# Kernel optimization log

Measured on AMD Instinct MI355X. Metric: run time of the kernel, lower is better.

## Reference

```python
import jax, jax.numpy as jnp
import numpy as np

BATCH = 16384
EPS = 1e-5


def _pool22_sum(x):
    # 4 * AvgPool2d((2,2),stride 2) == sum over 2x2 blocks. x: [B,1,h,w]
    B, C, h, w = x.shape
    return x.reshape(B, C, h // 2, 2, w // 2, 2).sum(axis=(3, 5))


def _transform(img, ans):
    # img: [B,h,h]. Faithful port of `transfrom`: zero border rows/cols, then
    # 10 quadratic features per 2x2 patch, laid out as [B,1,k,10k] with last
    # axis index = patch_col*10 + feature.
    B, h, w = img.shape
    if ans in ('top_bottom', 'all'):
        m = jnp.ones((h, 1), img.dtype).at[0].set(0).at[-1].set(0)
        img = img * m
    if ans in ('left_right', 'all'):
        m = jnp.ones((1, w), img.dtype).at[:, 0].set(0).at[:, -1].set(0)
        img = img * m
    k = h // 2
    p = img.reshape(B, k, 2, k, 2)
    b00 = p[:, :, 0, :, 0]; b01 = p[:, :, 0, :, 1]
    b10 = p[:, :, 1, :, 0]; b11 = p[:, :, 1, :, 1]
    prods = jnp.stack([
        b00 * b00, b01 * b01, b10 * b10, b11 * b11,
        b00 * b01, b00 * b10, b00 * b11,
        b01 * b10, b01 * b11, b10 * b11], axis=-1)  # [B,k,k,10]
    return prods.reshape(B, 1, k, 10 * k)


def _pool110_sum(a):
    # 10 * AvgPool2d((1,10),stride(1,10)) == sum over groups of 10 on last axis
    B, C, k, tk = a.shape
    return a.reshape(B, C, k, tk // 10, 10).sum(-1)


def _bn(x, gamma, beta):
    # BatchNorm2d(1) in training mode: batch stats over (N,H,W), biased var
    m = x.mean(axis=(0, 2, 3), keepdims=True)
    v = jnp.mean((x - m) ** 2, axis=(0, 2, 3), keepdims=True)
    g = gamma.reshape(1, -1, 1, 1)
    b = beta.reshape(1, -1, 1, 1)
    return (x - m) * jax.lax.rsqrt(v + EPS) * g + b


def setup_inputs() -> dict:
    key = jax.random.key(0)
    ks = jax.random.split(key, 16)

    def xavier(k, shape):
        fan_in, fan_out = shape[-1], shape[-2]
        std = np.sqrt(2.0 / (fan_in + fan_out))
        return jax.random.normal(k, shape, jnp.float32) * std

    return {
        'x': jax.random.normal(ks[0], (BATCH, 1, 28, 28), jnp.float32),
        'l1_w1': xavier(ks[1], (1, 28, 28)),
        'l1_w2_1': xavier(ks[2], (1, 14, 140)),
        'l1_w2_2': xavier(ks[3], (1, 14, 140)),
        'l1_w2_3': xavier(ks[4], (1, 14, 140)),
        'l1_w2_4': xavier(ks[5], (1, 14, 140)),
        'l1_w3': xavier(ks[6], (1, 14, 14)),
        'l2_w1': xavier(ks[7], (1, 14, 14)),
        'l2_w2': xavier(ks[8], (1, 7, 70)),
        'l2_w4': xavier(ks[9], (1, 7, 7)),
        'w_fc1': jax.random.normal(ks[10], (10, 49), jnp.float32) / np.sqrt(49.0),
        'b_fc1': jnp.zeros((10,), jnp.float32),
        'w_fc2': jax.random.normal(ks[11], (10, 2401), jnp.float32) / np.sqrt(2401.0),
        'b_fc2': jnp.zeros((10,), jnp.float32),
        'bn_gamma': jnp.ones((1,), jnp.float32),
        'bn_beta': jnp.zeros((1,), jnp.float32),
    }


def reference(x, l1_w1, l1_w2_1, l1_w2_2, l1_w2_3, l1_w2_4, l1_w3,
              l2_w1, l2_w2, l2_w4, w_fc1, b_fc1, w_fc2, b_fc2,
              bn_gamma, bn_beta):
    B = x.shape[0]
    img = x[:, 0]  # [B,28,28]
    # layer 1
    l1 = _pool22_sum(x * l1_w1)
    for W, ans in ((l1_w2_1, 'left_right'), (l1_w2_2, 'top_bottom'),
                   (l1_w2_3, 'all'), (l1_w2_4, 'none')):
        l1 = l1 + _pool110_sum(_transform(img, ans) * W)
    l1 = l1 + l1_w3  # [B,1,14,14]
    h = _bn(l1, bn_gamma, bn_beta)
    # layer 2
    l2 = _pool22_sum(h * l2_w1) + _pool110_sum(_transform(h[:, 0], 'none') * l2_w2) + l2_w4
    h = _bn(l2, bn_gamma, bn_beta)  # [B,1,7,7]
    # layer 3
    l3_x1 = h.reshape(B, -1) @ w_fc1.T + b_fc1
    v = h.reshape(B, 49)
    c = jnp.triu(v[:, :, None] * v[:, None, :])  # [B,49,49], trans_all_rg
    l3_x2 = c.reshape(B, -1) @ w_fc2.T + b_fc2
    return l3_x1 + l3_x2
```

## Files before the change

kernel.cpp:

```cpp
#include <hip/hip_runtime.h>

#define BATCH 16384
#define N1 (BATCH * 196)
#define N2 (BATCH * 49)
#define S1 8

#define WS_P1_OFF   0
#define WS_P2_OFF   32768
#define WS_W2S_OFF  65536
#define WS_L1G_OFF  262144
#define WS_L2G_OFF  6684672

__device__ __forceinline__ unsigned short f2bf(float f) {
    unsigned u = __float_as_uint(f);
    unsigned r = (u + 0x7FFFu + ((u >> 16) & 1u)) >> 16;
    return (unsigned short)r;
}
__device__ __forceinline__ float bf2f(unsigned short h) {
    return __uint_as_float((unsigned)h << 16);
}

__global__ void __launch_bounds__(256) k1(
        const float* __restrict__ x,
        const float* __restrict__ l1w1, const float* __restrict__ wA,
        const float* __restrict__ wB, const float* __restrict__ wC,
        const float* __restrict__ wD, const float* __restrict__ l1w3,
        const float* __restrict__ wf2, const float* __restrict__ wfc1,
        const float* __restrict__ bfc1, const float* __restrict__ bfc2,
        unsigned short* __restrict__ l1g, double* __restrict__ partials1,
        float* __restrict__ w2s) {
    __shared__ __align__(16) float xs[S1 * 784];
    __shared__ float wls[4], wlss[4];
    int t = threadIdx.x;

    const float4* src = (const float4*)(x + (size_t)blockIdx.x * (S1 * 784));
    float4 rbuf[6];
    #pragma unroll
    for (int i = 0; i < 6; ++i) rbuf[i] = src[t + 256 * i];
    float4 rtail;
    if (t < 32) rtail = src[t + 1536];

    bool active = t < 196;
    int pos = active ? t : 0;
    int pi = pos / 14, pj = pos - 14 * pi;
    int r0 = (2 * pi) * 28 + 2 * pj;
    float4 a0, a1, a2, a3;
    {
        float2 wt = *(const float2*)(l1w1 + r0);
        float2 wb = *(const float2*)(l1w1 + r0 + 28);
        a0 = make_float4(wt.x, wt.y, wb.x, wb.y);
        float mA0 = (pj != 0) ? 1.f : 0.f, mA1 = (pj != 13) ? 1.f : 0.f;
        float mB0 = (pi != 0) ? 1.f : 0.f, mB1 = (pi != 13) ? 1.f : 0.f;
        float eA[4] = {mA0, mA1, mA0, mA1};
        float eB[4] = {mB0, mB0, mB1, mB1};
        const int e1i[10] = {0,1,2,3,0,0,0,1,1,2};
        const int e2i[10] = {0,1,2,3,1,2,3,2,3,3};
        int wo = pi * 140 + 10 * pj;
        float wq[10];
        #pragma unroll
        for (int k = 0; k < 10; ++k) {
            float ca = eA[e1i[k]] * eA[e2i[k]];
            float cb = eB[e1i[k]] * eB[e2i[k]];
            wq[k] = wA[wo + k] * ca + wB[wo + k] * cb
                  + wC[wo + k] * ca * cb + wD[wo + k];
        }
        a1 = make_float4(wq[0], wq[1], wq[2], wq[3]);
        a2 = make_float4(wq[4], wq[5], wq[6], wq[7]);
        a3 = make_float4(wq[8], wq[9], l1w3[pos], 0.f);
    }

    float4* dst = (float4*)xs;
    #pragma unroll
    for (int i = 0; i < 6; ++i) dst[t + 256 * i] = rbuf[i];
    if (t < 32) dst[t + 1536] = rtail;
    __syncthreads();

    float accs[S1];
    float sum = 0.f, sumsq = 0.f;
    #pragma unroll
    for (int s = 0; s < S1; ++s) {
        const float* xb = xs + s * 784;
        float2 tp = *(const float2*)(xb + r0);
        float2 bo = *(const float2*)(xb + r0 + 28);
        float b00 = tp.x, b01 = tp.y, b10 = bo.x, b11 = bo.y;
        float acc = b00 * a0.x + b01 * a0.y + b10 * a0.z + b11 * a0.w;
        acc += b00 * b00 * a1.x + b01 * b01 * a1.y + b10 * b10 * a1.z + b11 * b11 * a1.w;
        acc += b00 * b01 * a2.x + b00 * b10 * a2.y + b00 * b11 * a2.z + b01 * b10 * a2.w;
        acc += b01 * b11 * a3.x + b10 * b11 * a3.y + a3.z;
        accs[s] = acc;
        if (active) { sum += acc; sumsq += acc * acc; }
    }

    __syncthreads();
    unsigned short* ob = (unsigned short*)xs;
    if (active) {
        int g = ((pi >> 1) * 7 + (pj >> 1)) * 4 + (pi & 1) * 2 + (pj & 1);
        #pragma unroll
        for (int s = 0; s < S1; ++s) ob[s * 196 + g] = f2bf(accs[s]);
    }
    __syncthreads();
    const unsigned int* ob32 = (const unsigned int*)ob;
    unsigned int* gout = (unsigned int*)(l1g + (size_t)blockIdx.x * (S1 * 196));
    #pragma unroll
    for (int r2 = 0; r2 < 3; ++r2) gout[t + 256 * r2] = ob32[t + 256 * r2];
    if (t < 16) gout[t + 768] = ob32[t + 768];

    #pragma unroll
    for (int off = 32; off; off >>= 1) {
        sum += __shfl_down(sum, off);
        sumsq += __shfl_down(sumsq, off);
    }
    int lane = t & 63, wid = t >> 6;
    if (lane == 0) { wls[wid] = sum; wlss[wid] = sumsq; }
    __syncthreads();
    if (t == 0) {
        partials1[blockIdx.x * 2]     = (double)(wls[0] + wls[1] + wls[2] + wls[3]);
        partials1[blockIdx.x * 2 + 1] = (double)(wlss[0] + wlss[1] + wlss[2] + wlss[3]);
    }

    if (blockIdx.x < 10) {
        int e = blockIdx.x * 256 + t;
        if (e < 2500) {
            int p = e / 50, q = e - 50 * p;
            float w[10];
            if (p < 49 && q < 49) {
                int lo = p < q ? p : q, hi = p < q ? q : p;
                float sc = (p == q) ? 1.f : 0.5f;
                #pragma unroll
                for (int o = 0; o < 10; ++o) w[o] = wf2[o * 2401 + lo * 49 + hi] * sc;
            } else if (p == 49 && q < 49) {
                #pragma unroll
                for (int o = 0; o < 10; ++o) w[o] = wfc1[o * 49 + q];
            } else if (p < 49) {
                #pragma unroll
                for (int o = 0; o < 10; ++o) w[o] = 0.f;
            } else {
                #pragma unroll
                for (int o = 0; o < 10; ++o) w[o] = bfc1[o] + bfc2[o];
            }
            #pragma unroll
            for (int o = 0; o < 10; ++o) w2s[e * 10 + o] = w[o];
        }
    }
}

__global__ void __launch_bounds__(256) k2(
        const unsigned short* __restrict__ l1g,
        const float* __restrict__ l2w1, const float* __restrict__ l2w2,
        const float* __restrict__ l2w4,
        const float* __restrict__ gamma, const float* __restrict__ beta,
        const double* __restrict__ partials1, double* __restrict__ partials2,
        float* __restrict__ l2g) {
    __shared__ float wls[4], wlss[4];
    __shared__ double dred[8];
    __shared__ float bcast[2];
    int t = threadIdx.x;
    int lane = t & 63, wid = t >> 6;
    int sbase = blockIdx.x * S1;

    bool active = t < 196;
    int tt = active ? t : 0;
    int sub = tt / 49;
    int pos = tt - 49 * sub;

    ushort4 u0 = *(const ushort4*)(l1g + ((size_t)(sbase + sub) * 49 + pos) * 4);
    ushort4 u1 = *(const ushort4*)(l1g + ((size_t)(sbase + 4 + sub) * 49 + pos) * 4);

    {
        double s = 0.0, ss = 0.0;
        const double* p1 = partials1 + t * 16;
        #pragma unroll
        for (int k = 0; k < 8; ++k) { s += p1[k * 2]; ss += p1[k * 2 + 1]; }
        #pragma unroll
        for (int off = 32; off; off >>= 1) {
            s += __shfl_down(s, off);
            ss += __shfl_down(ss, off);
        }
        if (lane == 0) { dred[wid * 2] = s; dred[wid * 2 + 1] = ss; }
        __syncthreads();
        if (t == 0) {
            double S = dred[0] + dred[2] + dred[4] + dred[6];
            double SS = dred[1] + dred[3] + dred[5] + dred[7];
            double mean = S / (double)N1;
            double var = SS / (double)N1 - mean * mean;
            float a = (float)((double)gamma[0] / sqrt(var + 1e-5));
            bcast[0] = a;
            bcast[1] = beta[0] - (float)mean * a;
        }
    }

    int pi = pos / 7, pj = pos - 7 * pi;
    int r0 = (2 * pi) * 14 + 2 * pj;
    float4 a0 = make_float4(l2w1[r0], l2w1[r0 + 1], l2w1[r0 + 14], l2w1[r0 + 15]);
    int wo = pi * 70 + 10 * pj;
    float4 q1 = make_float4(l2w2[wo],     l2w2[wo + 1], l2w2[wo + 2], l2w2[wo + 3]);
    float4 q2 = make_float4(l2w2[wo + 4], l2w2[wo + 5], l2w2[wo + 6], l2w2[wo + 7]);
    float4 q3 = make_float4(l2w2[wo + 8], l2w2[wo + 9], l2w4[pos], 0.f);
    __syncthreads();
    float a1 = bcast[0], c1 = bcast[1];

    float sum = 0.f, sumsq = 0.f;
    #pragma unroll
    for (int s2 = 0; s2 < 2; ++s2) {
        ushort4 u = s2 ? u1 : u0;
        int smp = sbase + s2 * 4 + sub;
        float h00 = fmaf(a1, bf2f(u.x), c1), h01 = fmaf(a1, bf2f(u.y), c1);
        float h10 = fmaf(a1, bf2f(u.z), c1), h11 = fmaf(a1, bf2f(u.w), c1);
        float acc = h00 * a0.x + h01 * a0.y + h10 * a0.z + h11 * a0.w;
        acc += h00 * h00 * q1.x + h01 * h01 * q1.y + h10 * h10 * q1.z + h11 * h11 * q1.w;
        acc += h00 * h01 * q2.x + h00 * h10 * q2.y + h00 * h11 * q2.z + h01 * h10 * q2.w;
        acc += h01 * h11 * q3.x + h10 * h11 * q3.y + q3.z;
        if (active) {
            l2g[(size_t)smp * 52 + pos] = acc;
            sum += acc;
            sumsq += acc * acc;
        }
    }

    #pragma unroll
    for (int off = 32; off; off >>= 1) {
        sum += __shfl_down(sum, off);
        sumsq += __shfl_down(sumsq, off);
    }
    if (lane == 0) { wls[wid] = sum; wlss[wid] = sumsq; }
    __syncthreads();
    if (t == 0) {
        partials2[blockIdx.x * 2]     = (double)(wls[0] + wls[1] + wls[2] + wls[3]);
        partials2[blockIdx.x * 2 + 1] = (double)(wlss[0] + wlss[1] + wlss[2] + wlss[3]);
    }
}

__global__ void __launch_bounds__(1024) k3(
        const float* __restrict__ l2g, const float* __restrict__ w2s,
        const float* __restrict__ gamma, const float* __restrict__ beta,
        const double* __restrict__ partials2, float* __restrict__ out) {
    __shared__ float part[16][64][10];
    __shared__ double dred[32];
    __shared__ float bcast[2];
    int t = threadIdx.x, lane = t & 63, wid = t >> 6;
    int s = blockIdx.x * 64 + lane;

    float v[52];
    const float4* vsrc = (const float4*)(l2g + (size_t)s * 52);
    #pragma unroll
    for (int k = 0; k < 13; ++k) *(float4*)(v + 4 * k) = vsrc[k];

    {
        const double* p2 = partials2 + t * 4;
        double sd = p2[0] + p2[2], ssd = p2[1] + p2[3];
        #pragma unroll
        for (int off = 32; off; off >>= 1) {
            sd += __shfl_down(sd, off);
            ssd += __shfl_down(ssd, off);
        }
        if (lane == 0) { dred[wid * 2] = sd; dred[wid * 2 + 1] = ssd; }
        __syncthreads();
        if (t == 0) {
            double S = 0.0, SS = 0.0;
            #pragma unroll
            for (int w = 0; w < 16; ++w) { S += dred[w * 2]; SS += dred[w * 2 + 1]; }
            double mean = S / (double)N2;
            double var = SS / (double)N2 - mean * mean;
            float a = (float)((double)gamma[0] / sqrt(var + 1e-5));
            bcast[0] = a;
            bcast[1] = beta[0] - (float)mean * a;
        }
        __syncthreads();
    }
    float a2 = bcast[0], c2 = bcast[1];
    #pragma unroll
    for (int k = 0; k < 49; ++k) v[k] = fmaf(a2, v[k], c2);
    v[49] = 1.f;

    float acc[10];
    #pragma unroll
    for (int o = 0; o < 10; ++o) acc[o] = 0.f;

    int W = __builtin_amdgcn_readfirstlane(wid);
    for (int r = W; r < 50; r += 16) {
        float vp = (r < 49) ? fmaf(a2, l2g[(size_t)s * 52 + r], c2) : 1.f;
        const float* wr = w2s + r * 500;
        #pragma unroll
        for (int q = 0; q < 50; ++q) {
            float c = vp * v[q];
            #pragma unroll
            for (int o = 0; o < 10; ++o) acc[o] = fmaf(c, wr[q * 10 + o], acc[o]);
        }
    }

    #pragma unroll
    for (int o = 0; o < 10; ++o) part[wid][lane][o] = acc[o];
    __syncthreads();

    if (t < 640) {
        int sl = t / 10, o = t - 10 * sl;
        float r2 = 0.f;
        #pragma unroll
        for (int w = 0; w < 16; ++w) r2 += part[w][sl][o];
        out[(size_t)(blockIdx.x * 64 + sl) * 10 + o] = r2;
    }
}

extern "C" void kernel_launch(void* const* d_in, const int* in_sizes, int n_in,
                              void* d_out, int out_size, void* d_ws, size_t ws_size,
                              hipStream_t stream) {
    const float* x       = (const float*)d_in[0];
    const float* l1_w1   = (const float*)d_in[1];
    const float* l1_w2_1 = (const float*)d_in[2];
    const float* l1_w2_2 = (const float*)d_in[3];
    const float* l1_w2_3 = (const float*)d_in[4];
    const float* l1_w2_4 = (const float*)d_in[5];
    const float* l1_w3   = (const float*)d_in[6];
    const float* l2_w1   = (const float*)d_in[7];
    const float* l2_w2   = (const float*)d_in[8];
    const float* l2_w4   = (const float*)d_in[9];
    const float* w_fc1   = (const float*)d_in[10];
    const float* b_fc1   = (const float*)d_in[11];
    const float* w_fc2   = (const float*)d_in[12];
    const float* b_fc2   = (const float*)d_in[13];
    const float* bn_gamma = (const float*)d_in[14];
    const float* bn_beta  = (const float*)d_in[15];

    char* ws = (char*)d_ws;
    double* partials1 = (double*)(ws + WS_P1_OFF);
    double* partials2 = (double*)(ws + WS_P2_OFF);
    float* w2s = (float*)(ws + WS_W2S_OFF);
    unsigned short* l1g = (unsigned short*)(ws + WS_L1G_OFF);
    float* l2g = (float*)(ws + WS_L2G_OFF);
    float* out = (float*)d_out;

    k1<<<BATCH / S1, 256, 0, stream>>>(x, l1_w1, l1_w2_1, l1_w2_2, l1_w2_3, l1_w2_4,
                                       l1_w3, w_fc2, w_fc1, b_fc1, b_fc2,
                                       l1g, partials1, w2s);
    k2<<<BATCH / S1, 256, 0, stream>>>(l1g, l2_w1, l2_w2, l2_w4, bn_gamma, bn_beta,
                                       partials1, partials2, l2g);
    k3<<<BATCH / 64, 1024, 0, stream>>>(l2g, w2s, bn_gamma, bn_beta, partials2, out);
}
```

Measured before the change: 48.34 us.

## Use upper-triangular pair stream with compile-time indices in FC2 kernel

The FC2 quadratic layer previously iterated over a full symmetrized 50x50 pair matrix (with halved off-diagonal weights plus a bias row and column). It now iterates only the 1225 upper-triangular (p,q) pairs, with weights pre-packed per wave into a contiguous stream. The pair indices are resolved at compile time via templates, so each wave indexes registers statically. FC1 and the bias are handled separately, removing roughly half of the FMAs. The cost is a 16-way switch over template instantiations that greatly enlarges code size, which may pressure the instruction cache.

```diff
diff --git a/kernel.cpp b/kernel.cpp
--- a/kernel.cpp
+++ b/kernel.cpp
@@ -4,12 +4,14 @@
 #define N1 (BATCH * 196)
 #define N2 (BATCH * 49)
 #define S1 8
-
-#define WS_P1_OFF   0
-#define WS_P2_OFF   32768
-#define WS_W2S_OFF  65536
-#define WS_L1G_OFF  262144
-#define WS_L2G_OFF  6684672
+#define NPART 16
+
+#define WS_P1_OFF    0
+#define WS_P2_OFF    32768
+#define WS_WSTR_OFF  65536
+#define WS_WFC1S_OFF 114816
+#define WS_L1G_OFF   262144
+#define WS_L2G_OFF   6684672
 
 __device__ __forceinline__ unsigned short f2bf(float f) {
     unsigned u = __float_as_uint(f);
@@ -18,6 +20,17 @@
 }
 __device__ __forceinline__ float bf2f(unsigned short h) {
     return __uint_as_float((unsigned)h << 16);
+}
+
+__host__ __device__ constexpr int pair_p(int i) {
+    int p = 0, rem = i;
+    while (rem >= 49 - p) { rem -= 49 - p; ++p; }
+    return p;
+}
+__host__ __device__ constexpr int pair_q(int i) {
+    int p = 0, rem = i;
+    while (rem >= 49 - p) { rem -= 49 - p; ++p; }
+    return p + rem;
 }
 
 __global__ void __launch_bounds__(256) k1(
@@ -26,9 +39,8 @@
         const float* __restrict__ wB, const float* __restrict__ wC,
         const float* __restrict__ wD, const float* __restrict__ l1w3,
         const float* __restrict__ wf2, const float* __restrict__ wfc1,
-        const float* __restrict__ bfc1, const float* __restrict__ bfc2,
         unsigned short* __restrict__ l1g, double* __restrict__ partials1,
-        float* __restrict__ w2s) {
+        float* __restrict__ wstream, float* __restrict__ wfc1s) {
     __shared__ __align__(16) float xs[S1 * 784];
     __shared__ float wls[4], wlss[4];
     int t = threadIdx.x;
@@ -120,26 +132,17 @@
 
     if (blockIdx.x < 10) {
         int e = blockIdx.x * 256 + t;
-        if (e < 2500) {
-            int p = e / 50, q = e - 50 * p;
-            float w[10];
-            if (p < 49 && q < 49) {
-                int lo = p < q ? p : q, hi = p < q ? q : p;
-                float sc = (p == q) ? 1.f : 0.5f;
-                #pragma unroll
-                for (int o = 0; o < 10; ++o) w[o] = wf2[o * 2401 + lo * 49 + hi] * sc;
-            } else if (p == 49 && q < 49) {
-                #pragma unroll
-                for (int o = 0; o < 10; ++o) w[o] = wfc1[o * 49 + q];
-            } else if (p < 49) {
-                #pragma unroll
-                for (int o = 0; o < 10; ++o) w[o] = 0.f;
-            } else {
-                #pragma unroll
-                for (int o = 0; o < 10; ++o) w[o] = bfc1[o] + bfc2[o];
-            }
+        if (e < 1225) {
+            int rem = e, p = 0;
+            while (rem >= 49 - p) { rem -= 49 - p; ++p; }
+            int q = p + rem;
+            int slot = ((e & (NPART - 1)) * 77 + (e / NPART)) * 10;
             #pragma unroll
-            for (int o = 0; o < 10; ++o) w2s[e * 10 + o] = w[o];
+            for (int o = 0; o < 10; ++o) wstream[slot + o] = wf2[o * 2401 + p * 49 + q];
+        } else if (e < 1274) {
+            int k = e - 1225;
+            #pragma unroll
+            for (int o = 0; o < 10; ++o) wfc1s[k * 10 + o] = wfc1[o * 49 + k];
         }
     }
 }
@@ -230,11 +233,43 @@
     }
 }
 
+template<int W, int J>
+__device__ __forceinline__ void fc2_steps(const float* __restrict__ wb,
+                                          const float* v, float* acc) {
+    constexpr int i = J * NPART + W;
+    if constexpr (i < 1225) {
+        constexpr int p = pair_p(i);
+        constexpr int q = pair_q(i);
+        float pv = v[p] * v[q];
+        const float* w = wb + J * 10;
+        #pragma unroll
+        for (int o = 0; o < 10; ++o) acc[o] = fmaf(pv, w[o], acc[o]);
+        fc2_steps<W, J + 1>(wb, v, acc);
+    }
+}
+
+template<int W>
+__device__ __forceinline__ void fc_all(const float* __restrict__ wstream,
+                                       const float* __restrict__ wfc1s,
+                                       const float* v, float* acc) {
+    #pragma unroll
+    for (int k = 0; k < 49; ++k) {
+        if ((k & (NPART - 1)) == W) {
+            const float* w = wfc1s + k * 10;
+            #pragma unroll
+            for (int o = 0; o < 10; ++o) acc[o] = fmaf(v[k], w[o], acc[o]);
+        }
+    }
+    fc2_steps<W, 0>(wstream + W * 770, v, acc);
+}
+
 __global__ void __launch_bounds__(1024) k3(
-        const float* __restrict__ l2g, const float* __restrict__ w2s,
+        const float* __restrict__ l2g, const float* __restrict__ wstream,
+        const float* __restrict__ wfc1s,
+        const float* __restrict__ b_fc1, const float* __restrict__ b_fc2,
         const float* __restrict__ gamma, const float* __restrict__ beta,
         const double* __restrict__ partials2, float* __restrict__ out) {
-    __shared__ float part[16][64][10];
+    __shared__ float part[NPART][64][10];
     __shared__ double dred[32];
     __shared__ float bcast[2];
     int t = threadIdx.x, lane = t & 63, wid = t >> 6;
@@ -270,22 +305,29 @@
     float a2 = bcast[0], c2 = bcast[1];
     #pragma unroll
     for (int k = 0; k < 49; ++k) v[k] = fmaf(a2, v[k], c2);
-    v[49] = 1.f;
 
     float acc[10];
     #pragma unroll
     for (int o = 0; o < 10; ++o) acc[o] = 0.f;
 
     int W = __builtin_amdgcn_readfirstlane(wid);
-    for (int r = W; r < 50; r += 16) {
-        float vp = (r < 49) ? fmaf(a2, l2g[(size_t)s * 52 + r], c2) : 1.f;
-        const float* wr = w2s + r * 500;
-        #pragma unroll
-        for (int q = 0; q < 50; ++q) {
-            float c = vp * v[q];
-            #pragma unroll
-            for (int o = 0; o < 10; ++o) acc[o] = fmaf(c, wr[q * 10 + o], acc[o]);
-        }
+    switch (W) {
+        case 0:  fc_all<0>(wstream, wfc1s, v, acc); break;
+        case 1:  fc_all<1>(wstream, wfc1s, v, acc); break;
+        case 2:  fc_all<2>(wstream, wfc1s, v, acc); break;
+        case 3:  fc_all<3>(wstream, wfc1s, v, acc); break;
+        case 4:  fc_all<4>(wstream, wfc1s, v, acc); break;
+        case 5:  fc_all<5>(wstream, wfc1s, v, acc); break;
+        case 6:  fc_all<6>(wstream, wfc1s, v, acc); break;
+        case 7:  fc_all<7>(wstream, wfc1s, v, acc); break;
+        case 8:  fc_all<8>(wstream, wfc1s, v, acc); break;
+        case 9:  fc_all<9>(wstream, wfc1s, v, acc); break;
+        case 10: fc_all<10>(wstream, wfc1s, v, acc); break;
+        case 11: fc_all<11>(wstream, wfc1s, v, acc); break;
+        case 12: fc_all<12>(wstream, wfc1s, v, acc); break;
+        case 13: fc_all<13>(wstream, wfc1s, v, acc); break;
+        case 14: fc_all<14>(wstream, wfc1s, v, acc); break;
+        default: fc_all<15>(wstream, wfc1s, v, acc); break;
     }
 
     #pragma unroll
@@ -296,8 +338,8 @@
         int sl = t / 10, o = t - 10 * sl;
         float r2 = 0.f;
         #pragma unroll
-        for (int w = 0; w < 16; ++w) r2 += part[w][sl][o];
-        out[(size_t)(blockIdx.x * 64 + sl) * 10 + o] = r2;
+        for (int w = 0; w < NPART; ++w) r2 += part[w][sl][o];
+        out[(size_t)(blockIdx.x * 64 + sl) * 10 + o] = r2 + b_fc1[o] + b_fc2[o];
     }
 }
 
@@ -324,15 +366,17 @@
     char* ws = (char*)d_ws;
     double* partials1 = (double*)(ws + WS_P1_OFF);
     double* partials2 = (double*)(ws + WS_P2_OFF);
-    float* w2s = (float*)(ws + WS_W2S_OFF);
+    float* wstream = (float*)(ws + WS_WSTR_OFF);
+    float* wfc1s   = (float*)(ws + WS_WFC1S_OFF);
     unsigned short* l1g = (unsigned short*)(ws + WS_L1G_OFF);
     float* l2g = (float*)(ws + WS_L2G_OFF);
     float* out = (float*)d_out;
 
     k1<<<BATCH / S1, 256, 0, stream>>>(x, l1_w1, l1_w2_1, l1_w2_2, l1_w2_3, l1_w2_4,
-                                       l1_w3, w_fc2, w_fc1, b_fc1, b_fc2,
-                                       l1g, partials1, w2s);
+                                       l1_w3, w_fc2, w_fc1, l1g, partials1,
+                                       wstream, wfc1s);
     k2<<<BATCH / S1, 256, 0, stream>>>(l1g, l2_w1, l2_w2, l2_w4, bn_gamma, bn_beta,
                                        partials1, partials2, l2g);
-    k3<<<BATCH / 64, 1024, 0, stream>>>(l2g, w2s, bn_gamma, bn_beta, partials2, out);
-}
+    k3<<<BATCH / 64, 1024, 0, stream>>>(l2g, wstream, wfc1s, b_fc1, b_fc2,
+                                        bn_gamma, bn_beta, partials2, out);
+}
```

New measurement: 51.39 us, median of 2. +6.3%, slower.

## Exploit upper-triangular structure in FC2 with packed pair records and LDS activations

Applied to the files above, without the earlier changes.

Replaces the dense 50x50 symmetric weight sweep in k3 with a list of 1274 upper-triangle (p,q) pair records, each holding 10 weights plus precomputed LDS offsets, split round-robin across 16 waves. Per-sample normalized activations now sit in shared memory in a transposed layout rather than in 52 registers. This roughly halves the FMA work and cuts register pressure. In exchange it adds two LDS reads and scalar readfirstlane loads per record, and moves the bias add to the final output write.

```diff
diff --git a/kernel.cpp b/kernel.cpp
--- a/kernel.cpp
+++ b/kernel.cpp
@@ -4,12 +4,13 @@
 #define N1 (BATCH * 196)
 #define N2 (BATCH * 49)
 #define S1 8
-
-#define WS_P1_OFF   0
-#define WS_P2_OFF   32768
-#define WS_W2S_OFF  65536
-#define WS_L1G_OFF  262144
-#define WS_L2G_OFF  6684672
+#define NREC 80
+
+#define WS_P1_OFF    0
+#define WS_P2_OFF    32768
+#define WS_WREC_OFF  65536
+#define WS_L1G_OFF   262144
+#define WS_L2G_OFF   6684672
 
 __device__ __forceinline__ unsigned short f2bf(float f) {
     unsigned u = __float_as_uint(f);
@@ -18,6 +19,9 @@
 }
 __device__ __forceinline__ float bf2f(unsigned short h) {
     return __uint_as_float((unsigned)h << 16);
+}
+__device__ __forceinline__ float rfl_f(float v) {
+    return __uint_as_float(__builtin_amdgcn_readfirstlane(__float_as_uint(v)));
 }
 
 __global__ void __launch_bounds__(256) k1(
@@ -26,9 +30,8 @@
         const float* __restrict__ wB, const float* __restrict__ wC,
         const float* __restrict__ wD, const float* __restrict__ l1w3,
         const float* __restrict__ wf2, const float* __restrict__ wfc1,
-        const float* __restrict__ bfc1, const float* __restrict__ bfc2,
         unsigned short* __restrict__ l1g, double* __restrict__ partials1,
-        float* __restrict__ w2s) {
+        float* __restrict__ wrec) {
     __shared__ __align__(16) float xs[S1 * 784];
     __shared__ float wls[4], wlss[4];
     int t = threadIdx.x;
@@ -118,28 +121,34 @@
         partials1[blockIdx.x * 2 + 1] = (double)(wlss[0] + wlss[1] + wlss[2] + wlss[3]);
     }
 
-    if (blockIdx.x < 10) {
+    if (blockIdx.x < 5) {
         int e = blockIdx.x * 256 + t;
-        if (e < 2500) {
-            int p = e / 50, q = e - 50 * p;
-            float w[10];
-            if (p < 49 && q < 49) {
-                int lo = p < q ? p : q, hi = p < q ? q : p;
-                float sc = (p == q) ? 1.f : 0.5f;
+        if (e < 1280) {
+            int w = e / NREC, j = e - w * NREC;
+            int i = j * 16 + w;
+            float wv[10];
+            int ip = 0, iq = 0;
+            if (i < 1225) {
+                int rem = i, p = 0;
+                while (rem >= 49 - p) { rem -= 49 - p; ++p; }
+                int q = p + rem;
                 #pragma unroll
-                for (int o = 0; o < 10; ++o) w[o] = wf2[o * 2401 + lo * 49 + hi] * sc;
-            } else if (p == 49 && q < 49) {
+                for (int o = 0; o < 10; ++o) wv[o] = wf2[o * 2401 + p * 49 + q];
+                ip = p * 64; iq = q * 64;
+            } else if (i < 1274) {
+                int k = i - 1225;
                 #pragma unroll
-                for (int o = 0; o < 10; ++o) w[o] = wfc1[o * 49 + q];
-            } else if (p < 49) {
-                #pragma unroll
-                for (int o = 0; o < 10; ++o) w[o] = 0.f;
+                for (int o = 0; o < 10; ++o) wv[o] = wfc1[o * 49 + k];
+                ip = k * 64; iq = 49 * 64;
             } else {
                 #pragma unroll
-                for (int o = 0; o < 10; ++o) w[o] = bfc1[o] + bfc2[o];
+                for (int o = 0; o < 10; ++o) wv[o] = 0.f;
             }
+            float* r = wrec + (size_t)e * 12;
             #pragma unroll
-            for (int o = 0; o < 10; ++o) w2s[e * 10 + o] = w[o];
+            for (int o = 0; o < 10; ++o) r[o] = wv[o];
+            ((int*)r)[10] = ip;
+            ((int*)r)[11] = iq;
         }
     }
 }
@@ -231,19 +240,23 @@
 }
 
 __global__ void __launch_bounds__(1024) k3(
-        const float* __restrict__ l2g, const float* __restrict__ w2s,
+        const float* __restrict__ l2g, const float* __restrict__ wrec,
+        const float* __restrict__ b_fc1, const float* __restrict__ b_fc2,
         const float* __restrict__ gamma, const float* __restrict__ beta,
         const double* __restrict__ partials2, float* __restrict__ out) {
     __shared__ float part[16][64][10];
+    __shared__ float vsm[50 * 64];
     __shared__ double dred[32];
     __shared__ float bcast[2];
     int t = threadIdx.x, lane = t & 63, wid = t >> 6;
-    int s = blockIdx.x * 64 + lane;
-
-    float v[52];
-    const float4* vsrc = (const float4*)(l2g + (size_t)s * 52);
-    #pragma unroll
-    for (int k = 0; k < 13; ++k) *(float4*)(v + 4 * k) = vsrc[k];
+
+    float4 val;
+    int vs_s = 0, vs_k4 = 0;
+    if (t < 832) {
+        vs_s = t / 13;
+        vs_k4 = t - vs_s * 13;
+        val = ((const float4*)(l2g + (size_t)blockIdx.x * 64 * 52))[vs_s * 13 + vs_k4];
+    }
 
     {
         const double* p2 = partials2 + t * 4;
@@ -268,24 +281,32 @@
         __syncthreads();
     }
     float a2 = bcast[0], c2 = bcast[1];
-    #pragma unroll
-    for (int k = 0; k < 49; ++k) v[k] = fmaf(a2, v[k], c2);
-    v[49] = 1.f;
+
+    if (t < 832) {
+        float vv[4] = {val.x, val.y, val.z, val.w};
+        #pragma unroll
+        for (int j = 0; j < 4; ++j) {
+            int p = vs_k4 * 4 + j;
+            if (p < 49) vsm[p * 64 + vs_s] = fmaf(a2, vv[j], c2);
+        }
+    }
+    if (t < 64) vsm[49 * 64 + t] = 1.f;
+    __syncthreads();
 
     float acc[10];
     #pragma unroll
     for (int o = 0; o < 10; ++o) acc[o] = 0.f;
 
     int W = __builtin_amdgcn_readfirstlane(wid);
-    for (int r = W; r < 50; r += 16) {
-        float vp = (r < 49) ? fmaf(a2, l2g[(size_t)s * 52 + r], c2) : 1.f;
-        const float* wr = w2s + r * 500;
-        #pragma unroll
-        for (int q = 0; q < 50; ++q) {
-            float c = vp * v[q];
-            #pragma unroll
-            for (int o = 0; o < 10; ++o) acc[o] = fmaf(c, wr[q * 10 + o], acc[o]);
-        }
+    const float* base = wrec + (size_t)W * NREC * 12;
+    #pragma unroll 4
+    for (int j = 0; j < NREC; ++j) {
+        const float* rec = base + j * 12;
+        int ip = __builtin_amdgcn_readfirstlane(((const int*)rec)[10]);
+        int iq = __builtin_amdgcn_readfirstlane(((const int*)rec)[11]);
+        float pv = vsm[ip + lane] * vsm[iq + lane];
+        #pragma unroll
+        for (int o = 0; o < 10; ++o) acc[o] = fmaf(pv, rfl_f(rec[o]), acc[o]);
     }
 
     #pragma unroll
@@ -297,7 +318,7 @@
         float r2 = 0.f;
         #pragma unroll
         for (int w = 0; w < 16; ++w) r2 += part[w][sl][o];
-        out[(size_t)(blockIdx.x * 64 + sl) * 10 + o] = r2;
+        out[(size_t)(blockIdx.x * 64 + sl) * 10 + o] = r2 + b_fc1[o] + b_fc2[o];
     }
 }
 
@@ -324,15 +345,15 @@
     char* ws = (char*)d_ws;
     double* partials1 = (double*)(ws + WS_P1_OFF);
     double* partials2 = (double*)(ws + WS_P2_OFF);
-    float* w2s = (float*)(ws + WS_W2S_OFF);
+    float* wrec = (float*)(ws + WS_WREC_OFF);
     unsigned short* l1g = (unsigned short*)(ws + WS_L1G_OFF);
     float* l2g = (float*)(ws + WS_L2G_OFF);
     float* out = (float*)d_out;
 
     k1<<<BATCH / S1, 256, 0, stream>>>(x, l1_w1, l1_w2_1, l1_w2_2, l1_w2_3, l1_w2_4,
-                                       l1_w3, w_fc2, w_fc1, b_fc1, b_fc2,
-                                       l1g, partials1, w2s);
+                                       l1_w3, w_fc2, w_fc1, l1g, partials1, wrec);
     k2<<<BATCH / S1, 256, 0, stream>>>(l1g, l2_w1, l2_w2, l2_w4, bn_gamma, bn_beta,
                                        partials1, partials2, l2g);
-    k3<<<BATCH / 64, 1024, 0, stream>>>(l2g, w2s, bn_gamma, bn_beta, partials2, out);
-}
+    k3<<<BATCH / 64, 1024, 0, stream>>>(l2g, wrec, b_fc1, b_fc2,
+                                        bn_gamma, bn_beta, partials2, out);
+}
```

Result: faster. 42.88 us (-11.3%).
